# Performance work log

Measured on AMD Instinct MI355X. Metric: run time of the kernel, lower is better.

The kernel has to match this reference:

```python
import jax, jax.numpy as jnp
import numpy as np

B, L, D, N, NBLK = 16, 2048, 256, 64, 6  # 6 S4D layers: blocks 1,2,3,5 + 2 inner layers of FS4Ddeq


def setup_inputs() -> dict:
    key = jax.random.key(0)
    ks = jax.random.split(key, 12)
    x = jax.random.normal(ks[0], (B, L), dtype=jnp.float32)
    W_emb = jax.random.normal(ks[1], (1, D), dtype=jnp.float32) * 0.1
    b_emb = jnp.zeros((D,), jnp.float32)
    # S4D parameters, stacked over the 6 layers
    log_dt = jax.random.uniform(ks[2], (NBLK, D), minval=float(np.log(1e-3)), maxval=float(np.log(1e-1)), dtype=jnp.float32)
    logAre = jnp.full((NBLK, D, N), float(np.log(0.5)), jnp.float32)
    Aim = jnp.broadcast_to(jnp.pi * jnp.arange(N, dtype=jnp.float32), (NBLK, D, N)) * jnp.ones((NBLK, D, N), jnp.float32)
    Cre = jax.random.normal(ks[3], (NBLK, D, N), dtype=jnp.float32) * (0.5 ** 0.5)
    Cim = jax.random.normal(ks[4], (NBLK, D, N), dtype=jnp.float32) * (0.5 ** 0.5)
    Dskip = jax.random.normal(ks[5], (NBLK, D), dtype=jnp.float32)
    Wout = jax.random.normal(ks[6], (NBLK, D, D), dtype=jnp.float32) / np.sqrt(D)
    bout = jnp.zeros((NBLK, D), jnp.float32)
    gamma = jnp.ones((NBLK, D), jnp.float32)
    beta = jnp.zeros((NBLK, D), jnp.float32)
    # feedforward of the FS4Ddeq block (feed_size=[B,L,emb_dim], feed_act='relu')
    feed_W1 = jax.random.normal(ks[7], (D, D), dtype=jnp.float32) / np.sqrt(D)
    feed_b1 = jnp.zeros((D,), jnp.float32)
    feed_W2 = jax.random.normal(ks[8], (D, D), dtype=jnp.float32) / np.sqrt(D)
    feed_b2 = jnp.zeros((D,), jnp.float32)
    fc_W = jax.random.normal(ks[9], (D, 2), dtype=jnp.float32) / np.sqrt(D)
    fc_b = jnp.zeros((2,), jnp.float32)
    return dict(x=x, W_emb=W_emb, b_emb=b_emb, log_dt=log_dt, logAre=logAre, Aim=Aim,
                Cre=Cre, Cim=Cim, Dskip=Dskip, Wout=Wout, bout=bout, gamma=gamma, beta=beta,
                feed_W1=feed_W1, feed_b1=feed_b1, feed_W2=feed_W2, feed_b2=feed_b2,
                fc_W=fc_W, fc_b=fc_b)


def _s4d_block(h, log_dt, logAre, Aim, Cre, Cim, Dskip, Wout, bout, gamma, beta):
    """Pre-norm (BN eval-mode) -> diagonal SSM (ZOH, FFT conv) -> GELU -> Linear -> residual."""
    _, Lh, _ = h.shape
    z = gamma * h + beta  # BatchNorm in eval mode with identity running stats
    dt = jnp.exp(log_dt)[:, None]                      # [D,1]
    A = -jnp.exp(logAre) + 1j * Aim                    # [D,N] diagonal state matrix
    dtA = dt * A                                       # [D,N]
    C = (Cre + 1j * Cim) * (jnp.exp(dtA) - 1.0) / A    # ZOH-discretized C*B
    # Vandermonde kernel K[d,l] = 2*Re sum_n C[d,n] * exp(dtA[d,n])^l
    vand = jnp.exp(dtA[:, :, None] * jnp.arange(Lh, dtype=jnp.float32))  # [D,N,L]
    K = 2.0 * jnp.einsum('dn,dnl->dl', C, vand).real   # [D,L]
    u = jnp.transpose(z, (0, 2, 1))                    # [B,D,L]
    kf = jnp.fft.rfft(K, n=2 * Lh)
    uf = jnp.fft.rfft(u, n=2 * Lh)
    y = jnp.fft.irfft(uf * kf, n=2 * Lh)[..., :Lh]     # causal conv
    y = y + Dskip[:, None] * u                         # feedthrough D
    y = jax.nn.gelu(jnp.transpose(y, (0, 2, 1)))       # [B,L,D]
    y = jnp.einsum('bld,de->ble', y, Wout) + bout      # output projection
    return y + h                                       # skip connection


def reference(x, W_emb, b_emb, log_dt, logAre, Aim, Cre, Cim, Dskip, Wout, bout,
              gamma, beta, feed_W1, feed_b1, feed_W2, feed_b2, fc_W, fc_b):
    h = x[..., None] @ W_emb + b_emb  # nn.Linear(1, emb_dim): [B,L,D]
    # layers 1,2,3,5: S4D blocks (dropout is identity in eval mode)
    for i in range(4):
        h = _s4d_block(h, log_dt[i], logAre[i], Aim[i], Cre[i], Cim[i],
                       Dskip[i], Wout[i], bout[i], gamma[i], beta[i])
    # layer4: FS4Ddeq_model with layers=2 inner S4D blocks + relu feed net + final relu + skip
    r = h
    for i in (4, 5):
        h = _s4d_block(h, log_dt[i], logAre[i], Aim[i], Cre[i], Cim[i],
                       Dskip[i], Wout[i], bout[i], gamma[i], beta[i])
    h = jax.nn.relu(h @ feed_W1 + feed_b1) @ feed_W2 + feed_b2
    h = jax.nn.relu(h + r)
    mean_y = jnp.mean(h, axis=1)       # [B,D]
    logits = mean_y @ fc_W + fc_b      # [B,2]
    return logits
```

## Files before the change

kernel.cpp:

```cpp
#include <hip/hip_runtime.h>
#include <hip/hip_fp16.h>
#include <math.h>

#define B_ 16
#define L_ 2048
#define D_ 256
#define N_ 64
#define NBLK_ 6
#define LC_ 128
#define NC_ 16

typedef _Float16 half8 __attribute__((ext_vector_type(8)));
typedef float f32x4 __attribute__((ext_vector_type(4)));

__device__ __forceinline__ unsigned short f2h(float f) {
  _Float16 h = (_Float16)f;
  return *(unsigned short*)&h;
}
__device__ __forceinline__ float h2f(unsigned short u) {
  _Float16 h = *(_Float16*)&u;
  return (float)h;
}

__global__ __launch_bounds__(256) void prep_kernel(
    const float* __restrict__ x, const float* __restrict__ wemb,
    const float* __restrict__ bemb,
    const float* __restrict__ log_dt, const float* __restrict__ logAre,
    const float* __restrict__ Aim, const float* __restrict__ Cre,
    const float* __restrict__ Cim,
    const float* __restrict__ Wout, const float* __restrict__ fW1,
    const float* __restrict__ fW2,
    float* __restrict__ wbuf, float* __restrict__ c2buf,
    float* __restrict__ wlbuf, unsigned short* __restrict__ WT,
    unsigned short* __restrict__ H, unsigned short* __restrict__ UT,
    int* __restrict__ cnt) {
  __shared__ __align__(16) unsigned char ldsraw[17408];
  int bid = blockIdx.x;
  int tid = threadIdx.x;
  if (bid < 384) {
    if (bid == 0 && tid < 16) cnt[tid] = 0;
    int idx = bid * 256 + tid;
    if (idx < NBLK_ * D_ * N_) {
      int blk = idx >> 14;
      int rem = idx & 16383;
      int d = rem >> 6;
      int n = rem & 63;
      float dt   = expf(log_dt[blk * D_ + d]);
      float are  = -expf(logAre[idx]);
      float aim  = Aim[idx];
      float dtar = dt * are, dtai = dt * aim;
      float er = expf(dtar);
      float wr = er * cosf(dtai);
      float wi = er * sinf(dtai);
      float inv = 1.0f / (are * are + aim * aim);
      float wm1r = wr - 1.0f;
      float br = (wm1r * are + wi * aim) * inv;
      float bi2 = (wi * are - wm1r * aim) * inv;
      float crv = Cre[idx], civ = Cim[idx];
      float c2r = 2.0f * (crv * br - civ * bi2);
      float c2i = 2.0f * (crv * bi2 + civ * br);
      float eL = expf((float)LC_ * dtar);
      float angL = (float)LC_ * dtai;
      float* wb = wbuf + (size_t)((blk << 8) + d) * 128;
      wb[n] = wr; wb[64 + n] = wi;
      float* cb = c2buf + (size_t)((blk << 8) + d) * 128;
      cb[n] = c2r; cb[64 + n] = c2i;
      wlbuf[2 * idx] = eL * cosf(angL); wlbuf[2 * idx + 1] = eL * sinf(angL);
    }
  } else if (bid < 512) {
    float (*tile)[65] = (float (*)[65])ldsraw;
    int b2 = bid - 384;
    int wv = b2 >> 4;
    int tk = (b2 >> 2) & 3;
    int tn = b2 & 3;
    const float* src = (wv < 6) ? (Wout + (size_t)wv * 65536) : (wv == 6 ? fW1 : fW2);
    int r = tid >> 4;
    int c = (tid & 15) << 2;
    for (int rr = 0; rr < 64; rr += 16) {
      float4 v = *(const float4*)(src + (size_t)(tk * 64 + r + rr) * 256 + tn * 64 + c);
      tile[r + rr][c] = v.x; tile[r + rr][c + 1] = v.y;
      tile[r + rr][c + 2] = v.z; tile[r + rr][c + 3] = v.w;
    }
    __syncthreads();
    for (int rr = 0; rr < 64; rr += 16) {
      int n = r + rr;
      ushort4 o;
      o.x = f2h(tile[c + 0][n]); o.y = f2h(tile[c + 1][n]);
      o.z = f2h(tile[c + 2][n]); o.w = f2h(tile[c + 3][n]);
      *(ushort4*)(WT + (size_t)wv * 65536 + (size_t)(tn * 64 + n) * 256 + tk * 64 + c) = o;
    }
  } else {
    unsigned short (*lds)[136] = (unsigned short (*)[136])ldsraw;
    int bi = bid - 512;
    int bc = bi >> 2, dq = bi & 3;
    int b = bc >> 4, ch = bc & 15;
    int tau0 = tid >> 4;
    int dl = (tid & 15) << 2;
    float w4[4], b4[4];
#pragma unroll
    for (int i = 0; i < 4; ++i) {
      w4[i] = wemb[dq * 64 + dl + i];
      b4[i] = bemb[dq * 64 + dl + i];
    }
    for (int tt = 0; tt < 128; tt += 16) {
      int l = ch * 128 + tt + tau0;
      float xv = x[b * L_ + l];
      ushort4 hv;
      hv.x = f2h(fmaf(xv, w4[0], b4[0]));
      hv.y = f2h(fmaf(xv, w4[1], b4[1]));
      hv.z = f2h(fmaf(xv, w4[2], b4[2]));
      hv.w = f2h(fmaf(xv, w4[3], b4[3]));
      lds[dl + 0][tt + tau0] = hv.x;
      lds[dl + 1][tt + tau0] = hv.y;
      lds[dl + 2][tt + tau0] = hv.z;
      lds[dl + 3][tt + tau0] = hv.w;
      *(ushort4*)(H + ((size_t)(b * L_ + l)) * D_ + dq * 64 + dl) = hv;
    }
    __syncthreads();
    int r = tid >> 2, seg = (tid & 3) << 5;
    unsigned short* dst = UT + ((size_t)((dq * 64 + r) * 256 + bc)) * 128 + seg;
    const unsigned short* srow = &lds[r][seg];
    *(uint4*)(dst + 0)  = *(const uint4*)(srow + 0);
    *(uint4*)(dst + 8)  = *(const uint4*)(srow + 8);
    *(uint4*)(dst + 16) = *(const uint4*)(srow + 16);
    *(uint4*)(dst + 24) = *(const uint4*)(srow + 24);
  }
}

__global__ __launch_bounds__(512, 4) void scan_fused(
    const unsigned short* __restrict__ UT,
    const float* __restrict__ WB, const float* __restrict__ C2B,
    const float* __restrict__ WLB,
    const float* __restrict__ gamma_, const float* __restrict__ beta_,
    const float* __restrict__ dskip,
    unsigned short* __restrict__ GT, int blk) {
  __shared__ __align__(16) unsigned short SLl[128 * 136];
  __shared__ __align__(16) unsigned short Bm[128 * 136];
  __shared__ float wc[256];
  __shared__ float Kt[128];
  __shared__ float Pb[128];
  __shared__ float Sb[128];
  int bid = blockIdx.x;
  int d = bid >> 1;
  int hm = (bid & 1) << 7;
  int tid = threadIdx.x, lane = tid & 63, w = tid >> 6;
  int wm = w << 4;
  int cn = lane & 15, rq = lane >> 4;
  int ko = rq << 3;
  const unsigned short* Au = UT + ((size_t)d * 256 + hm) * 128;

  half8 afr[4];
#pragma unroll
  for (int kc2 = 0; kc2 < 4; ++kc2)
    afr[kc2] = *(const half8*)(Au + (size_t)(wm + cn) * 128 + (kc2 << 5) + ko);

  if (tid < 128) wc[tid] = WB[(size_t)((blk << 8) + d) * 128 + tid];
  else if (tid < 256) wc[tid] = C2B[(size_t)((blk << 8) + d) * 128 + (tid - 128)];
  __syncthreads();
  int n = tid & 63;
  float gd = gamma_[blk * D_ + d], bd = beta_[blk * D_ + d], dsk = dskip[blk * D_ + d];
  float wr = wc[n], wi = wc[64 + n];
  float c2r = wc[128 + n], c2i = wc[192 + n];
  float pr0, pi0;
  int j0 = w << 4;
  {
    float pr = 1.f, pi = 0.f, br = wr, bi = wi;
    int e = j0;
    while (e) {
      if (e & 1) { float tt = pr * br - pi * bi; pi = pr * bi + pi * br; pr = tt; }
      float t2 = br * br - bi * bi; bi = 2.f * br * bi; br = t2;
      e >>= 1;
    }
    pr0 = pr; pi0 = pi;
#pragma unroll 4
    for (int k2 = 0; k2 < 16; ++k2) {
      int j = j0 + k2;
      Bm[n * 136 + (127 - j)]        = f2h(gd * pr);
      Bm[(64 + n) * 136 + (127 - j)] = f2h(-gd * pi);
      float qr = pr * wr - pi * wi, qi = pr * wi + pi * wr;
      float kc = c2r * pr - c2i * pi;
#pragma unroll
      for (int off = 1; off < 64; off <<= 1) kc += __shfl_xor(kc, off);
      if (n == 0) Kt[j] = kc + (j == 0 ? dsk : 0.f);
      pr = qr; pi = qi;
    }
  }
  if (tid < 64) {
    const float* wlp = WLB + (((size_t)((blk << 8) + d)) * 64 + tid) * 2;
    float wlr = wlp[0], wli = wlp[1];
    float nr = wlr - 1.f, ni = wli;
    float dr2 = wc[tid] - 1.f, di = wc[64 + tid];
    float iv = 1.f / (dr2 * dr2 + di * di);
    Sb[tid]      = bd * ((nr * dr2 + ni * di) * iv);
    Sb[64 + tid] = bd * (-((ni * dr2 - nr * di) * iv));
  }
  __syncthreads();

  {
    f32x4 acc[8];
#pragma unroll
    for (int a = 0; a < 8; ++a) acc[a] = (f32x4){0.f, 0.f, 0.f, 0.f};
    __builtin_amdgcn_s_setprio(1);
#pragma unroll
    for (int kc = 0; kc < 4; ++kc) {
#pragma unroll
      for (int nf = 0; nf < 8; ++nf) {
        half8 bf = *(const half8*)((const _Float16*)Bm + ((nf << 4) + cn) * 136 + (kc << 5) + ko);
        acc[nf] = __builtin_amdgcn_mfma_f32_16x16x32_f16(afr[kc], bf, acc[nf], 0, 0, 0);
      }
    }
    __builtin_amdgcn_s_setprio(0);
#pragma unroll
    for (int nf = 0; nf < 8; ++nf) {
      int nl = (nf << 4) + cn;
      float sb = Sb[nl];
#pragma unroll
      for (int rr = 0; rr < 4; ++rr) {
        int row = wm + (rq << 2) + rr;
        SLl[row * 136 + nl] = f2h(acc[nf][rr] + sb);
      }
    }
  }
  __syncthreads();

  {
    float pr = pr0, pi = pi0;
#pragma unroll 4
    for (int k2 = 0; k2 < 16; ++k2) {
      int j = j0 + k2;
      float qr = pr * wr - pi * wi, qi = pr * wi + pi * wr;
      Bm[j * 136 + n]      = f2h(c2r * qr - c2i * qi);
      Bm[j * 136 + 64 + n] = f2h(c2r * qi + c2i * qr);
      pr = qr; pi = qi;
    }
  }
  if (tid < 128) {
    float ps = 0.f;
    for (int t2 = 0; t2 <= tid; ++t2) ps += Kt[t2];
    Pb[tid] = bd * ps;
  }
  {
    int b = tid >> 6, nn = tid & 63;
    const float* wlp = WLB + (((size_t)((blk << 8) + d)) * 64 + nn) * 2;
    float wlr = wlp[0], wli = wlp[1];
    float Sr = 0.f, Sj = 0.f;
    int row0 = b << 4;
    float tr2 = h2f(SLl[row0 * 136 + nn]);
    float tj2 = h2f(SLl[row0 * 136 + 64 + nn]);
    for (int c = 0; c < NC_; ++c) {
      int row = row0 + c;
      float ntr = 0.f, ntj = 0.f;
      if (c < NC_ - 1) {
        ntr = h2f(SLl[(row + 1) * 136 + nn]);
        ntj = h2f(SLl[(row + 1) * 136 + 64 + nn]);
      }
      SLl[row * 136 + nn]      = f2h(Sr);
      SLl[row * 136 + 64 + nn] = f2h(Sj);
      float nSr = fmaf(wlr, Sr, fmaf(wli, Sj, tr2));
      Sj = fmaf(-wli, Sr, fmaf(wlr, Sj, tj2));
      Sr = nSr;
      tr2 = ntr; tj2 = ntj;
    }
  }
  __syncthreads();

  f32x4 acc3[8];
#pragma unroll
  for (int a = 0; a < 8; ++a) acc3[a] = (f32x4){0.f, 0.f, 0.f, 0.f};
  __builtin_amdgcn_s_setprio(1);
#pragma unroll
  for (int kc2 = 0; kc2 < 4; ++kc2) {
    int kc = kc2 << 5;
    half8 af = *(const half8*)((const _Float16*)SLl + (wm + cn) * 136 + kc + ko);
#pragma unroll
    for (int nf = 0; nf < 8; ++nf) {
      half8 bf = *(const half8*)((const _Float16*)Bm + ((nf << 4) + cn) * 136 + kc + ko);
      acc3[nf] = __builtin_amdgcn_mfma_f32_16x16x32_f16(af, bf, acc3[nf], 0, 0, 0);
    }
  }
  __builtin_amdgcn_s_setprio(0);
  __syncthreads();

  {
    int chunk = tid & 15, rg = tid >> 4;
#pragma unroll
    for (int it = 0; it < 4; ++it) {
      int trow = (it << 5) + rg;
      int tau0 = chunk << 3;
      unsigned short v[8];
#pragma unroll
      for (int i = 0; i < 8; ++i) {
        int tau = tau0 + i;
        v[i] = (tau <= trow) ? f2h(gd * Kt[trow - tau]) : (unsigned short)0;
      }
      *(uint4*)(Bm + (size_t)trow * 136 + tau0) = *(uint4*)v;
    }
  }
  __syncthreads();

  {
    __builtin_amdgcn_s_setprio(1);
#pragma unroll
    for (int kc2 = 0; kc2 < 4; ++kc2) {
#pragma unroll
      for (int nf = 0; nf < 8; ++nf) {
        half8 bf = *(const half8*)((const _Float16*)Bm + ((nf << 4) + cn) * 136 + (kc2 << 5) + ko);
        acc3[nf] = __builtin_amdgcn_mfma_f32_16x16x32_f16(afr[kc2], bf, acc3[nf], 0, 0, 0);
      }
    }
    __builtin_amdgcn_s_setprio(0);
#pragma unroll
    for (int nf = 0; nf < 8; ++nf) {
      int nl = (nf << 4) + cn;
      float pb2 = Pb[nl];
#pragma unroll
      for (int rr = 0; rr < 4; ++rr) {
        int ml = wm + (rq << 2) + rr;
        float xx = acc3[nf][rr] + pb2;
        float x3 = xx * xx * xx;
        float inner = 0.7978845608028654f * fmaf(0.044715f, x3, xx);
        float e = __expf(-2.f * fabsf(inner));
        float th = (1.f - e) / (1.f + e);
        th = copysignf(th, inner);
        SLl[ml * 136 + nl] = f2h(0.5f * xx * (1.f + th));
      }
    }
    __syncthreads();
    int mr = tid >> 2, hf = (tid & 3) << 5;
    size_t gb = ((size_t)d * 256 + hm + mr) * 128 + hf;
#pragma unroll
    for (int k = 0; k < 4; ++k)
      *(uint4*)(GT + gb + k * 8) = *(const uint4*)&SLl[mr * 136 + hf + k * 8];
  }
}

__global__ __launch_bounds__(256, 4) void gemm_gt(const unsigned short* __restrict__ GT,
    const unsigned short* __restrict__ Wt, const float* __restrict__ bias,
    const unsigned short* __restrict__ res, unsigned short* __restrict__ hout,
    unsigned short* __restrict__ ut_next) {
  __shared__ __align__(16) unsigned short smem[9216 + 4608];
  unsigned short* As = smem;
  unsigned short* Bs = smem + 9216;
  int tid = threadIdx.x;
  int bid = blockIdx.x;
  int bc = bid & 255;
  int m0 = bc << 7, n0 = (bid >> 8) << 6;
  int lane = tid & 63, w = tid >> 6;
  int wm = (w & 1) << 6, wn = (w >> 1) << 5;
  int rb = tid >> 3, cb = (tid & 7) << 3;
  int dr = tid >> 2, sg = (tid & 3) << 5;
  f32x4 acc[4][2];
#pragma unroll
  for (int mf = 0; mf < 4; ++mf)
#pragma unroll
    for (int nf = 0; nf < 2; ++nf) acc[mf][nf] = (f32x4){0.f, 0.f, 0.f, 0.f};

  uint4 gv[4], bv[2];
  {
    const uint4* grow = (const uint4*)(GT + ((size_t)(dr * 256 + bc)) * 128 + sg);
    gv[0] = grow[0]; gv[1] = grow[1]; gv[2] = grow[2]; gv[3] = grow[3];
#pragma unroll
    for (int rr = 0; rr < 2; ++rr)
      bv[rr] = *(const uint4*)(Wt + (size_t)(n0 + rb + rr * 32) * 256 + cb);
  }
  for (int kb = 0; kb < 4; ++kb) {
    __syncthreads();
    const unsigned short* pv = (const unsigned short*)gv;
#pragma unroll
    for (int i = 0; i < 32; ++i) As[(sg + i) * 72 + dr] = pv[i];
#pragma unroll
    for (int rr = 0; rr < 2; ++rr) *(uint4*)&Bs[(rb + rr * 32) * 72 + cb] = bv[rr];
    __syncthreads();
    if (kb < 3) {
      int k0 = (kb + 1) << 6;
      const uint4* grow = (const uint4*)(GT + ((size_t)((k0 + dr) * 256 + bc)) * 128 + sg);
      gv[0] = grow[0]; gv[1] = grow[1]; gv[2] = grow[2]; gv[3] = grow[3];
#pragma unroll
      for (int rr = 0; rr < 2; ++rr)
        bv[rr] = *(const uint4*)(Wt + (size_t)(n0 + rb + rr * 32) * 256 + k0 + cb);
    }
#pragma unroll
    for (int kw = 0; kw < 2; ++kw) {
      int ko = (kw << 5) + ((lane >> 4) << 3);
      half8 af[4], bfr[2];
#pragma unroll
      for (int mf = 0; mf < 4; ++mf)
        af[mf] = *(const half8*)&As[(wm + (mf << 4) + (lane & 15)) * 72 + ko];
#pragma unroll
      for (int nf = 0; nf < 2; ++nf)
        bfr[nf] = *(const half8*)&Bs[(wn + (nf << 4) + (lane & 15)) * 72 + ko];
#pragma unroll
      for (int mf = 0; mf < 4; ++mf)
#pragma unroll
        for (int nf = 0; nf < 2; ++nf)
          acc[mf][nf] = __builtin_amdgcn_mfma_f32_16x16x32_f16(af[mf], bfr[nf], acc[mf][nf], 0, 0, 0);
    }
  }
  int cn = lane & 15, rq = lane >> 4;
  __syncthreads();
  unsigned short* epi = smem;
#pragma unroll
  for (int nf = 0; nf < 2; ++nf) {
    int nl = wn + (nf << 4) + cn;
    float bv2 = bias[n0 + nl];
#pragma unroll
    for (int mf = 0; mf < 4; ++mf)
#pragma unroll
      for (int r = 0; r < 4; ++r) {
        int ml = wm + (mf << 4) + (rq << 2) + r;
        float v = acc[mf][nf][r] + bv2 + h2f(res[(size_t)(m0 + ml) * 256 + n0 + nl]);
        epi[ml * 72 + nl] = f2h(v);
      }
  }
  __syncthreads();
  {
    int mr = tid >> 1, hf = (tid & 1) << 5;
    unsigned short* dst = hout + (size_t)(m0 + mr) * 256 + n0 + hf;
    const unsigned short* srow = epi + mr * 72 + hf;
#pragma unroll
    for (int k = 0; k < 4; ++k) *(uint4*)(dst + k * 8) = *(const uint4*)(srow + k * 8);
  }
  if (ut_next) {
    int nl = tid >> 2, sg2 = (tid & 3) << 5;
    unsigned short* dst = ut_next + ((size_t)(n0 + nl) * 256 + bc) * 128 + sg2;
#pragma unroll
    for (int k = 0; k < 4; ++k) {
      unsigned short v8[8];
#pragma unroll
      for (int e = 0; e < 8; ++e) v8[e] = epi[(sg2 + k * 8 + e) * 72 + nl];
      *(uint4*)(dst + k * 8) = *(uint4*)v8;
    }
  }
}

__global__ __launch_bounds__(256, 4) void gemm_ffn(const unsigned short* __restrict__ A,
    const unsigned short* __restrict__ Wt, const float* __restrict__ bias,
    const unsigned short* __restrict__ res, unsigned short* __restrict__ outp) {
  __shared__ __align__(16) unsigned short smem[9216 + 4608];
  unsigned short* As = smem;
  unsigned short* Bs = smem + 9216;
  int tid = threadIdx.x;
  int bid = blockIdx.x;
  int m0 = (bid & 255) << 7, n0 = (bid >> 8) << 6;
  int lane = tid & 63, w = tid >> 6;
  int wm = (w & 1) << 6, wn = (w >> 1) << 5;
  int r0 = tid >> 3;
  int c0 = (tid & 7) << 3;
  f32x4 acc[4][2];
#pragma unroll
  for (int mf = 0; mf < 4; ++mf)
#pragma unroll
    for (int nf = 0; nf < 2; ++nf) acc[mf][nf] = (f32x4){0.f, 0.f, 0.f, 0.f};

  uint4 av[4], bv[2];
#pragma unroll
  for (int rr = 0; rr < 4; ++rr)
    av[rr] = *(const uint4*)(A + (size_t)(m0 + r0 + rr * 32) * 256 + c0);
#pragma unroll
  for (int rr = 0; rr < 2; ++rr)
    bv[rr] = *(const uint4*)(Wt + (size_t)(n0 + r0 + rr * 32) * 256 + c0);
  for (int kb = 0; kb < 4; ++kb) {
    __syncthreads();
#pragma unroll
    for (int rr = 0; rr < 4; ++rr) *(uint4*)&As[(r0 + rr * 32) * 72 + c0] = av[rr];
#pragma unroll
    for (int rr = 0; rr < 2; ++rr) *(uint4*)&Bs[(r0 + rr * 32) * 72 + c0] = bv[rr];
    __syncthreads();
    if (kb < 3) {
      int k0 = (kb + 1) << 6;
#pragma unroll
      for (int rr = 0; rr < 4; ++rr)
        av[rr] = *(const uint4*)(A + (size_t)(m0 + r0 + rr * 32) * 256 + k0 + c0);
#pragma unroll
      for (int rr = 0; rr < 2; ++rr)
        bv[rr] = *(const uint4*)(Wt + (size_t)(n0 + r0 + rr * 32) * 256 + k0 + c0);
    }
#pragma unroll
    for (int kw = 0; kw < 2; ++kw) {
      int ko = (kw << 5) + ((lane >> 4) << 3);
      half8 af[4], bfr[2];
#pragma unroll
      for (int mf = 0; mf < 4; ++mf)
        af[mf] = *(const half8*)&As[(wm + (mf << 4) + (lane & 15)) * 72 + ko];
#pragma unroll
      for (int nf = 0; nf < 2; ++nf)
        bfr[nf] = *(const half8*)&Bs[(wn + (nf << 4) + (lane & 15)) * 72 + ko];
#pragma unroll
      for (int mf = 0; mf < 4; ++mf)
#pragma unroll
        for (int nf = 0; nf < 2; ++nf)
          acc[mf][nf] = __builtin_amdgcn_mfma_f32_16x16x32_f16(af[mf], bfr[nf], acc[mf][nf], 0, 0, 0);
    }
  }
  int cn = lane & 15, rq = lane >> 4;
  __syncthreads();
  unsigned short* epi = smem;
#pragma unroll
  for (int nf = 0; nf < 2; ++nf) {
    int nl = wn + (nf << 4) + cn;
#pragma unroll
    for (int r = 0; r < 4; ++r) {
#pragma unroll
      for (int mf = 0; mf < 4; ++mf) {
        int ml = wm + (mf << 4) + (rq << 2) + r;
        epi[ml * 72 + nl] = f2h(acc[mf][nf][r]);
      }
    }
  }
  __syncthreads();
  int mr = tid >> 1, hf = (tid & 1) << 5;
  unsigned short* dst = outp + (size_t)(m0 + mr) * 256 + n0 + hf;
#pragma unroll
  for (int k = 0; k < 4; ++k) {
    uint4 c = *(const uint4*)&epi[mr * 72 + hf + k * 8];
    uint4 rv = (uint4){0, 0, 0, 0};
    if (res) rv = *(const uint4*)(res + (size_t)(m0 + mr) * 256 + n0 + hf + k * 8);
    const unsigned short* cp = (const unsigned short*)&c;
    const unsigned short* rp = (const unsigned short*)&rv;
    unsigned short o8[8];
#pragma unroll
    for (int e = 0; e < 8; ++e) {
      float v = h2f(cp[e]) + bias[n0 + hf + k * 8 + e];
      if (res) v += h2f(rp[e]);
      o8[e] = f2h(fmaxf(v, 0.f));
    }
    *(uint4*)(dst + k * 8) = *(uint4*)o8;
  }
}

__global__ __launch_bounds__(256) void head_kernel(const unsigned short* __restrict__ H,
    float* __restrict__ part, int* __restrict__ cnt,
    const float* __restrict__ fcW, const float* __restrict__ fcb,
    float* __restrict__ out) {
  __shared__ float meanv[D_];
  __shared__ int lastFlag;
  int b = blockIdx.x, ls = blockIdx.y, d = threadIdx.x;
  const unsigned short* p = H + ((size_t)(b * L_ + ls * 128)) * D_ + d;
  float sum = 0.f;
  for (int l = 0; l < 128; ++l) sum += h2f(p[(size_t)l * D_]);
  part[(b * 16 + ls) * D_ + d] = sum;
  __syncthreads();
  if (d == 0) {
    __threadfence();
    lastFlag = (atomicAdd(&cnt[b], 1) == 15) ? 1 : 0;
  }
  __syncthreads();
  if (lastFlag) {
    __threadfence();
    const volatile float* vp = part;
    float s = 0.f;
    for (int i = 0; i < 16; ++i) s += vp[(b * 16 + i) * D_ + d];
    meanv[d] = s * (1.0f / (float)L_);
    __syncthreads();
    if (d < 2) {
      float accv = fcb[d];
      for (int k = 0; k < D_; ++k) accv = fmaf(meanv[k], fcW[k * 2 + d], accv);
      out[b * 2 + d] = accv;
    }
  }
}

extern "C" void kernel_launch(void* const* d_in, const int* in_sizes, int n_in,
                              void* d_out, int out_size, void* d_ws, size_t ws_size,
                              hipStream_t stream) {
  const float* x      = (const float*)d_in[0];
  const float* W_emb  = (const float*)d_in[1];
  const float* b_emb  = (const float*)d_in[2];
  const float* log_dt = (const float*)d_in[3];
  const float* logAre = (const float*)d_in[4];
  const float* Aim    = (const float*)d_in[5];
  const float* Cre    = (const float*)d_in[6];
  const float* Cim    = (const float*)d_in[7];
  const float* Dskip  = (const float*)d_in[8];
  const float* Wout   = (const float*)d_in[9];
  const float* bout   = (const float*)d_in[10];
  const float* gamma_ = (const float*)d_in[11];
  const float* beta_  = (const float*)d_in[12];
  const float* fW1    = (const float*)d_in[13];
  const float* fb1    = (const float*)d_in[14];
  const float* fW2    = (const float*)d_in[15];
  const float* fb2    = (const float*)d_in[16];
  const float* fcW    = (const float*)d_in[17];
  const float* fcb    = (const float*)d_in[18];
  float* outp = (float*)d_out;

  const size_t HSZ = (size_t)B_ * L_ * D_;
  float* WB     = (float*)d_ws;
  float* C2B    = WB + (size_t)NBLK_ * D_ * 128;
  float* WLB    = C2B + (size_t)NBLK_ * D_ * 128;
  unsigned short* H   = (unsigned short*)(WLB + (size_t)NBLK_ * D_ * N_ * 2);
  unsigned short* R   = H + HSZ;
  unsigned short* UT  = R + HSZ;
  unsigned short* GT  = UT + HSZ;
  unsigned short* Gbf = GT;
  unsigned short* WT  = GT + HSZ;
  int* cnt = (int*)(WT + (size_t)8 * 65536);

  prep_kernel<<<1536, 256, 0, stream>>>(x, W_emb, b_emb, log_dt, logAre, Aim, Cre, Cim,
                                        Wout, fW1, fW2, WB, C2B, WLB, WT, H, UT, cnt);

  const unsigned short* hin_t[6]  = {H, H, H, H, R, H};
  unsigned short*       hout_t[6] = {H, H, H, R, H, H};
  for (int i = 0; i < 6; ++i) {
    scan_fused<<<512, 512, 0, stream>>>(UT, WB, C2B, WLB, gamma_, beta_, Dskip, GT, i);
    gemm_gt<<<1024, 256, 0, stream>>>(
        GT, WT + (size_t)i * 65536, bout + i * D_, hin_t[i], hout_t[i],
        (i < 5) ? UT : nullptr);
  }
  gemm_ffn<<<1024, 256, 0, stream>>>(H, WT + (size_t)6 * 65536, fb1, nullptr, Gbf);
  gemm_ffn<<<1024, 256, 0, stream>>>(Gbf, WT + (size_t)7 * 65536, fb2, R, H);
  head_kernel<<<dim3(16, 16), 256, 0, stream>>>(H, WB, cnt, fcW, fcb, outp);
}
```

Before: 552.1 us.

## Precompute per-channel SSM operator matrices once and split scan into smaller blocks

A new matgen kernel builds the per-layer, per-channel F, E and Toeplitz matrices plus the prefix and state bias vectors once for all six layers and stores them in global memory. Before this, every scan block rebuilt them for its own layer. scan_fused now reads those matrices straight from global memory as MFMA B operands, and runs 2048 blocks of 256 threads, each handling 32 rows instead of 128. This drops repeated matrix construction and redundant generation across the two half-blocks, but adds global and L2 traffic for the operator matrices and a larger workspace.

After: 736.5 us. 1.33x slower.

```diff
diff --git a/kernel.cpp b/kernel.cpp
--- a/kernel.cpp
+++ b/kernel.cpp
@@ -127,42 +127,24 @@
   }
 }
 
-__global__ __launch_bounds__(512, 4) void scan_fused(
-    const unsigned short* __restrict__ UT,
+__global__ __launch_bounds__(512, 2) void matgen(
     const float* __restrict__ WB, const float* __restrict__ C2B,
     const float* __restrict__ WLB,
     const float* __restrict__ gamma_, const float* __restrict__ beta_,
     const float* __restrict__ dskip,
-    unsigned short* __restrict__ GT, int blk) {
-  __shared__ __align__(16) unsigned short SLl[128 * 136];
-  __shared__ __align__(16) unsigned short Bm[128 * 136];
-  __shared__ float wc[256];
+    unsigned short* __restrict__ FnG, unsigned short* __restrict__ EnG,
+    unsigned short* __restrict__ TnG, float* __restrict__ PbG,
+    float* __restrict__ SbG) {
+  __shared__ __align__(16) unsigned short buf[128 * 136];
   __shared__ float Kt[128];
-  __shared__ float Pb[128];
-  __shared__ float Sb[128];
   int bid = blockIdx.x;
-  int d = bid >> 1;
-  int hm = (bid & 1) << 7;
-  int tid = threadIdx.x, lane = tid & 63, w = tid >> 6;
-  int wm = w << 4;
-  int cn = lane & 15, rq = lane >> 4;
-  int ko = rq << 3;
-  const unsigned short* Au = UT + ((size_t)d * 256 + hm) * 128;
-
-  half8 afr[4];
-#pragma unroll
-  for (int kc2 = 0; kc2 < 4; ++kc2)
-    afr[kc2] = *(const half8*)(Au + (size_t)(wm + cn) * 128 + (kc2 << 5) + ko);
-
-  if (tid < 128) wc[tid] = WB[(size_t)((blk << 8) + d) * 128 + tid];
-  else if (tid < 256) wc[tid] = C2B[(size_t)((blk << 8) + d) * 128 + (tid - 128)];
-  __syncthreads();
-  int n = tid & 63;
-  float gd = gamma_[blk * D_ + d], bd = beta_[blk * D_ + d], dsk = dskip[blk * D_ + d];
-  float wr = wc[n], wi = wc[64 + n];
-  float c2r = wc[128 + n], c2i = wc[192 + n];
+  int ld = bid;
+  int tid = threadIdx.x, w = tid >> 6, n = tid & 63;
+  float wr = WB[(size_t)ld * 128 + n], wi = WB[(size_t)ld * 128 + 64 + n];
+  float c2r = C2B[(size_t)ld * 128 + n], c2i = C2B[(size_t)ld * 128 + 64 + n];
+  float gd = gamma_[ld], bd = beta_[ld], dsk = dskip[ld];
+  int j0 = w << 4;
   float pr0, pi0;
-  int j0 = w << 4;
   {
     float pr = 1.f, pi = 0.f, br = wr, bi = wi;
     int e = j0;
@@ -172,83 +154,156 @@
       e >>= 1;
     }
     pr0 = pr; pi0 = pi;
+  }
+  {
+    float pr = pr0, pi = pi0;
 #pragma unroll 4
     for (int k2 = 0; k2 < 16; ++k2) {
       int j = j0 + k2;
-      Bm[n * 136 + (127 - j)]        = f2h(gd * pr);
-      Bm[(64 + n) * 136 + (127 - j)] = f2h(-gd * pi);
-      float qr = pr * wr - pi * wi, qi = pr * wi + pi * wr;
+      buf[n * 136 + (127 - j)]        = f2h(gd * pr);
+      buf[(64 + n) * 136 + (127 - j)] = f2h(-gd * pi);
       float kc = c2r * pr - c2i * pi;
 #pragma unroll
       for (int off = 1; off < 64; off <<= 1) kc += __shfl_xor(kc, off);
       if (n == 0) Kt[j] = kc + (j == 0 ? dsk : 0.f);
+      float qr = pr * wr - pi * wi, qi = pr * wi + pi * wr;
       pr = qr; pi = qi;
     }
   }
+  __syncthreads();
+  {
+    int r = tid >> 2, s = (tid & 3) << 5;
+    unsigned short* dst = FnG + ((size_t)ld << 14) + r * 128 + s;
+    const unsigned short* src = buf + r * 136 + s;
+#pragma unroll
+    for (int k = 0; k < 4; ++k) *(uint4*)(dst + k * 8) = *(const uint4*)(src + k * 8);
+  }
+  if (tid < 128) {
+    float ps = 0.f;
+    for (int t2 = 0; t2 <= tid; ++t2) ps += Kt[t2];
+    PbG[(size_t)ld * 128 + tid] = bd * ps;
+  }
   if (tid < 64) {
-    const float* wlp = WLB + (((size_t)((blk << 8) + d)) * 64 + tid) * 2;
+    const float* wlp = WLB + ((size_t)ld * 64 + n) * 2;
     float wlr = wlp[0], wli = wlp[1];
     float nr = wlr - 1.f, ni = wli;
-    float dr2 = wc[tid] - 1.f, di = wc[64 + tid];
+    float dr2 = wr - 1.f, di = wi;
     float iv = 1.f / (dr2 * dr2 + di * di);
-    Sb[tid]      = bd * ((nr * dr2 + ni * di) * iv);
-    Sb[64 + tid] = bd * (-((ni * dr2 - nr * di) * iv));
-  }
-  __syncthreads();
-
-  {
-    f32x4 acc[8];
-#pragma unroll
-    for (int a = 0; a < 8; ++a) acc[a] = (f32x4){0.f, 0.f, 0.f, 0.f};
-    __builtin_amdgcn_s_setprio(1);
-#pragma unroll
-    for (int kc = 0; kc < 4; ++kc) {
-#pragma unroll
-      for (int nf = 0; nf < 8; ++nf) {
-        half8 bf = *(const half8*)((const _Float16*)Bm + ((nf << 4) + cn) * 136 + (kc << 5) + ko);
-        acc[nf] = __builtin_amdgcn_mfma_f32_16x16x32_f16(afr[kc], bf, acc[nf], 0, 0, 0);
-      }
-    }
-    __builtin_amdgcn_s_setprio(0);
-#pragma unroll
-    for (int nf = 0; nf < 8; ++nf) {
-      int nl = (nf << 4) + cn;
-      float sb = Sb[nl];
-#pragma unroll
-      for (int rr = 0; rr < 4; ++rr) {
-        int row = wm + (rq << 2) + rr;
-        SLl[row * 136 + nl] = f2h(acc[nf][rr] + sb);
-      }
-    }
-  }
-  __syncthreads();
-
+    SbG[(size_t)ld * 128 + n]      = bd * ((nr * dr2 + ni * di) * iv);
+    SbG[(size_t)ld * 128 + 64 + n] = bd * (-((ni * dr2 - nr * di) * iv));
+  }
+  __syncthreads();
   {
     float pr = pr0, pi = pi0;
 #pragma unroll 4
     for (int k2 = 0; k2 < 16; ++k2) {
       int j = j0 + k2;
       float qr = pr * wr - pi * wi, qi = pr * wi + pi * wr;
-      Bm[j * 136 + n]      = f2h(c2r * qr - c2i * qi);
-      Bm[j * 136 + 64 + n] = f2h(c2r * qi + c2i * qr);
+      buf[j * 136 + n]      = f2h(c2r * qr - c2i * qi);
+      buf[j * 136 + 64 + n] = f2h(c2r * qi + c2i * qr);
       pr = qr; pi = qi;
     }
   }
+  __syncthreads();
+  {
+    int r = tid >> 2, s = (tid & 3) << 5;
+    unsigned short* dst = EnG + ((size_t)ld << 14) + r * 128 + s;
+    const unsigned short* src = buf + r * 136 + s;
+#pragma unroll
+    for (int k = 0; k < 4; ++k) *(uint4*)(dst + k * 8) = *(const uint4*)(src + k * 8);
+  }
+  __syncthreads();
+  {
+    int chunk = tid & 15, rg = tid >> 4;
+#pragma unroll
+    for (int it = 0; it < 4; ++it) {
+      int trow = (it << 5) + rg;
+      int tau0 = chunk << 3;
+      unsigned short v[8];
+#pragma unroll
+      for (int i = 0; i < 8; ++i) {
+        int tau = tau0 + i;
+        v[i] = (tau <= trow) ? f2h(gd * Kt[trow - tau]) : (unsigned short)0;
+      }
+      *(uint4*)(buf + (size_t)trow * 136 + tau0) = *(uint4*)v;
+    }
+  }
+  __syncthreads();
+  {
+    int r = tid >> 2, s = (tid & 3) << 5;
+    unsigned short* dst = TnG + ((size_t)ld << 14) + r * 128 + s;
+    const unsigned short* src = buf + r * 136 + s;
+#pragma unroll
+    for (int k = 0; k < 4; ++k) *(uint4*)(dst + k * 8) = *(const uint4*)(src + k * 8);
+  }
+}
+
+__global__ __launch_bounds__(256, 4) void scan_fused(
+    const unsigned short* __restrict__ UT,
+    const unsigned short* __restrict__ FnG, const unsigned short* __restrict__ EnG,
+    const unsigned short* __restrict__ TnG,
+    const float* __restrict__ PbG, const float* __restrict__ SbG,
+    const float* __restrict__ WLB,
+    unsigned short* __restrict__ GT, int blk) {
+  __shared__ __align__(16) unsigned short SLl[32 * 136];
+  __shared__ float PbS[128];
+  __shared__ float SbS[128];
+  int bid = blockIdx.x;
+  int d = bid >> 3, b2 = bid & 7;
+  int ld = (blk << 8) + d;
+  int row0 = b2 << 5;
+  int tid = threadIdx.x, lane = tid & 63, w = tid >> 6;
+  int mh = w & 1, ng = w >> 1;
+  int cn = lane & 15, rq = lane >> 4, ko = rq << 3;
+  const unsigned short* Au = UT + ((size_t)d * 256 + row0) * 128;
+  const unsigned short* Fb = FnG + ((size_t)ld << 14);
+  const unsigned short* Eb = EnG + ((size_t)ld << 14);
+  const unsigned short* Tb = TnG + ((size_t)ld << 14);
+
   if (tid < 128) {
-    float ps = 0.f;
-    for (int t2 = 0; t2 <= tid; ++t2) ps += Kt[t2];
-    Pb[tid] = bd * ps;
-  }
-  {
-    int b = tid >> 6, nn = tid & 63;
-    const float* wlp = WLB + (((size_t)((blk << 8) + d)) * 64 + nn) * 2;
+    PbS[tid] = PbG[(size_t)ld * 128 + tid];
+    SbS[tid] = SbG[(size_t)ld * 128 + tid];
+  }
+
+  half8 afr[4];
+#pragma unroll
+  for (int kc = 0; kc < 4; ++kc)
+    afr[kc] = *(const half8*)(Au + (size_t)((mh << 4) + cn) * 128 + (kc << 5) + ko);
+
+  f32x4 acc[4];
+#pragma unroll
+  for (int a = 0; a < 4; ++a) acc[a] = (f32x4){0.f, 0.f, 0.f, 0.f};
+#pragma unroll
+  for (int kc = 0; kc < 4; ++kc) {
+#pragma unroll
+    for (int nf = 0; nf < 4; ++nf) {
+      half8 bf = *(const half8*)(Fb + (size_t)((ng << 6) + (nf << 4) + cn) * 128 + (kc << 5) + ko);
+      acc[nf] = __builtin_amdgcn_mfma_f32_16x16x32_f16(afr[kc], bf, acc[nf], 0, 0, 0);
+    }
+  }
+  __syncthreads();
+#pragma unroll
+  for (int nf = 0; nf < 4; ++nf) {
+    int nl = (ng << 6) + (nf << 4) + cn;
+    float sb = SbS[nl];
+#pragma unroll
+    for (int rr = 0; rr < 4; ++rr) {
+      int row = (mh << 4) + (rq << 2) + rr;
+      SLl[row * 136 + nl] = f2h(acc[nf][rr] + sb);
+    }
+  }
+  __syncthreads();
+
+  if (tid < 128) {
+    int bb = tid >> 6, nn = tid & 63;
+    const float* wlp = WLB + ((size_t)ld * 64 + nn) * 2;
     float wlr = wlp[0], wli = wlp[1];
     float Sr = 0.f, Sj = 0.f;
-    int row0 = b << 4;
-    float tr2 = h2f(SLl[row0 * 136 + nn]);
-    float tj2 = h2f(SLl[row0 * 136 + 64 + nn]);
+    int r0c = bb << 4;
+    float tr2 = h2f(SLl[r0c * 136 + nn]);
+    float tj2 = h2f(SLl[r0c * 136 + 64 + nn]);
     for (int c = 0; c < NC_; ++c) {
-      int row = row0 + c;
+      int row = r0c + c;
       float ntr = 0.f, ntj = 0.f;
       if (c < NC_ - 1) {
         ntr = h2f(SLl[(row + 1) * 136 + nn]);
@@ -264,73 +319,50 @@
   }
   __syncthreads();
 
-  f32x4 acc3[8];
-#pragma unroll
-  for (int a = 0; a < 8; ++a) acc3[a] = (f32x4){0.f, 0.f, 0.f, 0.f};
-  __builtin_amdgcn_s_setprio(1);
-#pragma unroll
-  for (int kc2 = 0; kc2 < 4; ++kc2) {
-    int kc = kc2 << 5;
-    half8 af = *(const half8*)((const _Float16*)SLl + (wm + cn) * 136 + kc + ko);
-#pragma unroll
-    for (int nf = 0; nf < 8; ++nf) {
-      half8 bf = *(const half8*)((const _Float16*)Bm + ((nf << 4) + cn) * 136 + kc + ko);
+  f32x4 acc3[4];
+#pragma unroll
+  for (int a = 0; a < 4; ++a) acc3[a] = (f32x4){0.f, 0.f, 0.f, 0.f};
+#pragma unroll
+  for (int kc = 0; kc < 4; ++kc) {
+    half8 af = *(const half8*)((const _Float16*)SLl + (size_t)((mh << 4) + cn) * 136 + (kc << 5) + ko);
+#pragma unroll
+    for (int nf = 0; nf < 4; ++nf) {
+      half8 bf = *(const half8*)(Eb + (size_t)((ng << 6) + (nf << 4) + cn) * 128 + (kc << 5) + ko);
       acc3[nf] = __builtin_amdgcn_mfma_f32_16x16x32_f16(af, bf, acc3[nf], 0, 0, 0);
     }
   }
-  __builtin_amdgcn_s_setprio(0);
-  __syncthreads();
-
-  {
-    int chunk = tid & 15, rg = tid >> 4;
-#pragma unroll
-    for (int it = 0; it < 4; ++it) {
-      int trow = (it << 5) + rg;
-      int tau0 = chunk << 3;
-      unsigned short v[8];
-#pragma unroll
-      for (int i = 0; i < 8; ++i) {
-        int tau = tau0 + i;
-        v[i] = (tau <= trow) ? f2h(gd * Kt[trow - tau]) : (unsigned short)0;
-      }
-      *(uint4*)(Bm + (size_t)trow * 136 + tau0) = *(uint4*)v;
-    }
-  }
-  __syncthreads();
-
-  {
-    __builtin_amdgcn_s_setprio(1);
-#pragma unroll
-    for (int kc2 = 0; kc2 < 4; ++kc2) {
-#pragma unroll
-      for (int nf = 0; nf < 8; ++nf) {
-        half8 bf = *(const half8*)((const _Float16*)Bm + ((nf << 4) + cn) * 136 + (kc2 << 5) + ko);
-        acc3[nf] = __builtin_amdgcn_mfma_f32_16x16x32_f16(afr[kc2], bf, acc3[nf], 0, 0, 0);
-      }
-    }
-    __builtin_amdgcn_s_setprio(0);
-#pragma unroll
-    for (int nf = 0; nf < 8; ++nf) {
-      int nl = (nf << 4) + cn;
-      float pb2 = Pb[nl];
-#pragma unroll
-      for (int rr = 0; rr < 4; ++rr) {
-        int ml = wm + (rq << 2) + rr;
-        float xx = acc3[nf][rr] + pb2;
-        float x3 = xx * xx * xx;
-        float inner = 0.7978845608028654f * fmaf(0.044715f, x3, xx);
-        float e = __expf(-2.f * fabsf(inner));
-        float th = (1.f - e) / (1.f + e);
-        th = copysignf(th, inner);
-        SLl[ml * 136 + nl] = f2h(0.5f * xx * (1.f + th));
-      }
-    }
-    __syncthreads();
-    int mr = tid >> 2, hf = (tid & 3) << 5;
-    size_t gb = ((size_t)d * 256 + hm + mr) * 128 + hf;
-#pragma unroll
-    for (int k = 0; k < 4; ++k)
-      *(uint4*)(GT + gb + k * 8) = *(const uint4*)&SLl[mr * 136 + hf + k * 8];
+#pragma unroll
+  for (int kc = 0; kc < 4; ++kc) {
+#pragma unroll
+    for (int nf = 0; nf < 4; ++nf) {
+      half8 bf = *(const half8*)(Tb + (size_t)((ng << 6) + (nf << 4) + cn) * 128 + (kc << 5) + ko);
+      acc3[nf] = __builtin_amdgcn_mfma_f32_16x16x32_f16(afr[kc], bf, acc3[nf], 0, 0, 0);
+    }
+  }
+  __syncthreads();
+
+#pragma unroll
+  for (int nf = 0; nf < 4; ++nf) {
+    int nl = (ng << 6) + (nf << 4) + cn;
+    float pb2 = PbS[nl];
+#pragma unroll
+    for (int rr = 0; rr < 4; ++rr) {
+      int ml = (mh << 4) + (rq << 2) + rr;
+      float xx = acc3[nf][rr] + pb2;
+      float x3 = xx * xx * xx;
+      float inner = 0.7978845608028654f * fmaf(0.044715f, x3, xx);
+      float e = __expf(-2.f * fabsf(inner));
+      float th = (1.f - e) / (1.f + e);
+      th = copysignf(th, inner);
+      SLl[ml * 136 + nl] = f2h(0.5f * xx * (1.f + th));
+    }
+  }
+  __syncthreads();
+  {
+    int mr = tid >> 3, hb = (tid & 7) << 4;
+    unsigned short* dst = GT + ((size_t)d * 256 + row0 + mr) * 128 + hb;
+    *(uint4*)(dst + 0) = *(const uint4*)&SLl[mr * 136 + hb + 0];
+    *(uint4*)(dst + 8) = *(const uint4*)&SLl[mr * 136 + hb + 8];
   }
 }
 
@@ -585,6 +617,7 @@
   float* outp = (float*)d_out;
 
   const size_t HSZ = (size_t)B_ * L_ * D_;
+  const size_t MSZ = (size_t)NBLK_ * D_ * 128 * 128;
   float* WB     = (float*)d_ws;
   float* C2B    = WB + (size_t)NBLK_ * D_ * 128;
   float* WLB    = C2B + (size_t)NBLK_ * D_ * 128;
@@ -594,15 +627,22 @@
   unsigned short* GT  = UT + HSZ;
   unsigned short* Gbf = GT;
   unsigned short* WT  = GT + HSZ;
-  int* cnt = (int*)(WT + (size_t)8 * 65536);
+  unsigned short* FnG = WT + (size_t)8 * 65536;
+  unsigned short* EnG = FnG + MSZ;
+  unsigned short* TnG = EnG + MSZ;
+  float* PbG = (float*)(TnG + MSZ);
+  float* SbG = PbG + (size_t)NBLK_ * D_ * 128;
+  int* cnt = (int*)(SbG + (size_t)NBLK_ * D_ * 128);
 
   prep_kernel<<<1536, 256, 0, stream>>>(x, W_emb, b_emb, log_dt, logAre, Aim, Cre, Cim,
                                         Wout, fW1, fW2, WB, C2B, WLB, WT, H, UT, cnt);
+  matgen<<<NBLK_ * 256, 512, 0, stream>>>(WB, C2B, WLB, gamma_, beta_, Dskip,
+                                          FnG, EnG, TnG, PbG, SbG);
 
   const unsigned short* hin_t[6]  = {H, H, H, H, R, H};
   unsigned short*       hout_t[6] = {H, H, H, R, H, H};
   for (int i = 0; i < 6; ++i) {
-    scan_fused<<<512, 512, 0, stream>>>(UT, WB, C2B, WLB, gamma_, beta_, Dskip, GT, i);
+    scan_fused<<<2048, 256, 0, stream>>>(UT, FnG, EnG, TnG, PbG, SbG, WLB, GT, i);
     gemm_gt<<<1024, 256, 0, stream>>>(
         GT, WT + (size_t)i * 65536, bout + i * D_, hin_t[i], hout_t[i],
         (i < 5) ? UT : nullptr);
```
